# Kernel tuning notes

Measured on AMD Instinct MI355X. Metric: run time of the kernel, lower is better.

The kernel has to match this reference:

```python
import jax, jax.numpy as jnp
import numpy as np

GROUP_SIZE = 128

def setup_inputs() -> dict:
    key = jax.random.key(0)
    k0, k1, k2, k3 = jax.random.split(key, 4)
    B, S, K, N = 4, 16, 8192, 28672
    G = GROUP_SIZE
    x = jax.random.normal(k0, (B, S, K), dtype=jnp.float16)
    # packed uint8 stored as int32 (2 int4 nibbles per byte along K)
    w_packed = jax.random.randint(k1, (K // 2, N), 0, 256, dtype=jnp.int32)
    # per-group positive scales, typical magnitude for int4 quant of fp16 weights
    scales = (jax.random.uniform(k2, (K // G, N), dtype=jnp.float32) * 0.02 + 1e-4).astype(jnp.float16)
    bias = (jax.random.normal(k3, (N,), dtype=jnp.float16) * 0.02).astype(jnp.float16)
    return {"x": x, "w_packed": w_packed, "scales": scales, "bias": bias}

def _dequant(w_packed, scales):
    # w_packed: [K//2, N] ints in [0,256); low nibble -> even k, high nibble -> odd k
    low = (w_packed & 15) - 8          # [K//2, N] int32 in [-8, 7]
    high = ((w_packed >> 4) & 15) - 8  # [K//2, N]
    Kh, N = w_packed.shape
    w_int = jnp.stack([low, high], axis=1).reshape(Kh * 2, N)  # interleave -> [K, N]
    s = jnp.repeat(scales, GROUP_SIZE, axis=0)                 # [K, N] fp16
    return w_int.astype(jnp.float16) * s                       # [K, N] fp16

def reference(x, w_packed, scales, bias):
    # x: [B, S, K] fp16 -> y: [B, S, N] fp16
    w = _dequant(w_packed, scales)                 # [K, N] fp16
    lead = x.shape[:-1]
    x2 = x.reshape(-1, x.shape[-1])                # [M, K]
    # fp32 accumulation, fp16 output (matches Triton kernel's tl.dot accumulator)
    y = jnp.dot(x2, w, preferred_element_type=jnp.float32).astype(jnp.float16)
    y = y + bias
    return y.reshape(*lead, -1)
```

## Files before the change

### kernel.cpp

```cpp
#include <hip/hip_runtime.h>


typedef short  short8  __attribute__((ext_vector_type(8)));
typedef float  float4v __attribute__((ext_vector_type(4)));
typedef int    int4v   __attribute__((ext_vector_type(4)));
typedef unsigned int uint4v __attribute__((ext_vector_type(4)));

constexpr int Kd = 8192;
constexpr int Nd = 28672;
constexpr int KSPLIT = 4;

__device__ __forceinline__ unsigned f32_to_bf16_rn(float f) {
    unsigned u = __builtin_bit_cast(unsigned, f);
    return (u + 0x7FFFu + ((u >> 16) & 1u)) >> 16;
}

__device__ __forceinline__ void async16(const void* g, void* l) {
    __builtin_amdgcn_global_load_lds(
        (const __attribute__((address_space(1))) unsigned*)g,
        (__attribute__((address_space(3))) unsigned*)l, 16, 0, 0);
}

__global__ __launch_bounds__(256)
void init_y_kernel(const float* __restrict__ bias, float* __restrict__ y) {
    const int gid = blockIdx.x * 256 + threadIdx.x;
    const int m  = gid / (Nd / 4);
    const int nq = gid % (Nd / 4);
    ((float4v*)y)[(long)m * (Nd / 4) + nq] = ((const float4v*)bias)[nq];
}

__global__ __launch_bounds__(256)
void cvt_x_kernel(const float* __restrict__ x, unsigned short* __restrict__ o) {
    const int i = (blockIdx.x * 256 + threadIdx.x) * 8;
    float4v a = *(const float4v*)(x + i);
    float4v b = *(const float4v*)(x + i + 4);
    union { unsigned short s[8]; short8 v; } r;
    #pragma unroll
    for (int j = 0; j < 4; ++j) {
        r.s[j]     = (unsigned short)f32_to_bf16_rn(a[j]);
        r.s[4 + j] = (unsigned short)f32_to_bf16_rn(b[j]);
    }
    *(short8*)(o + i) = r.v;
}

__global__ __launch_bounds__(256, 4)
void int4_main_kernel(const unsigned short* __restrict__ xw,
                      const int*            __restrict__ wp,
                      const float*          __restrict__ scales,
                      float*                __restrict__ y)
{
    __shared__ unsigned wb0[2048], wb1[2048];
    __shared__ unsigned xb0[2048], xb1[2048];
    __shared__ unsigned sb[1024];

    const int t = threadIdx.x, lane = t & 63, wv = t >> 6;
    const int q = lane >> 4, c = lane & 15;
    const int l4 = lane >> 4, l15 = lane & 15;
    const int n0 = blockIdx.x * 64, kz = blockIdx.y;

    const int* wsrc0; const int* wsrc1;
    {
        int r0 = wv * 8 + 0 * 4 + l4, c0 = (l15 * 4) ^ (((wv * 2 + 0) & 3) << 4);
        int r1 = wv * 8 + 1 * 4 + l4, c1 = (l15 * 4) ^ (((wv * 2 + 1) & 3) << 4);
        wsrc0 = wp + (long)(kz * 1024 + r0) * Nd + n0 + c0;
        wsrc1 = wp + (long)(kz * 1024 + r1) * Nd + n0 + c1;
    }
    const unsigned short* xsrc0; const unsigned short* xsrc1;
    {
        int s0 = wv * 128 + 0 * 64 + lane, m0 = s0 >> 3, k0 = (s0 & 7) ^ (m0 & 7);
        int s1 = wv * 128 + 1 * 64 + lane, m1 = s1 >> 3, k1 = (s1 & 7) ^ (m1 & 7);
        xsrc0 = xw + (long)m0 * Kd + kz * 2048 + k0 * 8;
        xsrc1 = xw + (long)m1 * Kd + kz * 2048 + k1 * 8;
    }
    const int ldof = wv * 512;

    {
        const float* ssrc = scales + (long)(kz * 16 + (t >> 4)) * Nd + n0 + (t & 15) * 4;
        async16(ssrc, sb + wv * 256);
    }
    async16(wsrc0, wb0 + ldof);
    async16(wsrc1, wb0 + ldof + 256);
    async16(xsrc0, xb0 + ldof);
    async16(xsrc1, xb0 + ldof + 256);

    float4v acc[4] = {};

    auto stage = [&](int hg, unsigned* wbuf, unsigned* xbuf) {
        const long wof = (long)hg * 32 * Nd;
        const long xof = (long)hg * 64;
        async16(wsrc0 + wof, wbuf + ldof);
        async16(wsrc1 + wof, wbuf + ldof + 256);
        async16(xsrc0 + xof, xbuf + ldof);
        async16(xsrc1 + xof, xbuf + ldof + 256);
    };

    auto compute = [&](const unsigned* wbuf, const unsigned* xbuf, int g) {
        const float s   = __builtin_bit_cast(float, sb[g * 64 + wv * 16 + c]);
        const float m8s = -8.0f * s;
        #pragma unroll
        for (int it = 0; it < 2; ++it) {
            union { short8 h; unsigned u[4]; } bu;
            #pragma unroll
            for (int i = 0; i < 4; ++i) {
                unsigned v = wbuf[(it * 16 + q * 4 + i) * 64 + ((wv * 16 + c) ^ (q << 4))];
                float lo = fmaf((float)(v & 15u), s, m8s);
                float hi = fmaf((float)((v >> 4) & 15u), s, m8s);
                bu.u[i] = f32_to_bf16_rn(lo) | (f32_to_bf16_rn(hi) << 16);
            }
            #pragma unroll
            for (int mt = 0; mt < 4; ++mt) {
                int m = mt * 16 + c;
                int slot = m * 8 + ((it * 4 + q) ^ (c & 7));
                short8 a = *(const short8*)(xbuf + slot * 4);
                acc[mt] = __builtin_amdgcn_mfma_f32_16x16x32_bf16(a, bu.h, acc[mt], 0, 0, 0);
            }
        }
    };

    for (int hgp = 0; hgp < 16; ++hgp) {
        const int hg = 2 * hgp;
        stage(hg + 1, wb1, xb1);
        asm volatile("s_waitcnt vmcnt(4)\ns_barrier" ::: "memory");
        compute(wb0, xb0, hgp);
        asm volatile("s_waitcnt lgkmcnt(0)\ns_barrier" ::: "memory");
        if (hgp < 15) {
            stage(hg + 2, wb0, xb0);
            asm volatile("s_waitcnt vmcnt(4)\ns_barrier" ::: "memory");
        } else {
            asm volatile("s_waitcnt vmcnt(0)\ns_barrier" ::: "memory");
        }
        compute(wb1, xb1, hgp);
        asm volatile("s_waitcnt lgkmcnt(0)\ns_barrier" ::: "memory");
    }

    const int nw = n0 + wv * 16 + c;
    #pragma unroll
    for (int mt = 0; mt < 4; ++mt)
        #pragma unroll
        for (int r = 0; r < 4; ++r)
            atomicAdd(&y[(long)(mt * 16 + q * 4 + r) * Nd + nw], acc[mt][r]);
}

__global__ __launch_bounds__(256, 6)
void int4_main_nows_kernel(const float* __restrict__ xf,
                           const int*   __restrict__ wp,
                           const float* __restrict__ scales,
                           float*       __restrict__ y)
{
    constexpr int LDS_STRIDE = 68;
    __shared__ unsigned lds_w[64 * LDS_STRIDE];
    const int t = threadIdx.x, lane = t & 63, wv = t >> 6;
    const int q = lane >> 4, c = lane & 15;
    const int n0 = blockIdx.x * 64, kz = blockIdx.y;
    const int sr = t >> 4, ss = t & 15;
    const int*   wp_b = wp + (long)(kz * 1024 + sr) * Nd + n0 + 4 * ss;
    const float* sc_b = scales + (long)(kz * 16) * Nd + n0 + 4 * ss;
    const float* xf_b = xf + (long)c * Kd + kz * 2048 + q * 8;
    float4v acc[4] = {};

    for (int g = 0; g < 16; ++g) {
        const float4v s4 = *(const float4v*)(sc_b + (long)g * Nd);
        const int* wg = wp_b + (long)g * 64 * Nd;
        #pragma unroll
        for (int i = 0; i < 4; ++i) {
            int4v v = *(const int4v*)(wg + (long)i * 16 * Nd);
            uint4v pk;
            #pragma unroll
            for (int j = 0; j < 4; ++j) {
                float lo = (float)((v[j] & 15) - 8) * s4[j];
                float hi = (float)(((v[j] >> 4) & 15) - 8) * s4[j];
                pk[j] = f32_to_bf16_rn(lo) | (f32_to_bf16_rn(hi) << 16);
            }
            *(uint4v*)&lds_w[(i * 16 + sr) * LDS_STRIDE + 4 * ss] = pk;
        }
        __syncthreads();
        const float* xg = xf_b + g * 128;
        #pragma unroll
        for (int it = 0; it < 4; ++it) {
            union { short8 h; unsigned u[4]; } bu;
            #pragma unroll
            for (int i = 0; i < 4; ++i)
                bu.u[i] = lds_w[(it * 16 + q * 4 + i) * LDS_STRIDE + wv * 16 + c];
            const short8 b = bu.h;
            const float* xk = xg + it * 32;
            #pragma unroll
            for (int mt = 0; mt < 4; ++mt) {
                float4v a0 = *(const float4v*)(xk + (long)mt * 16 * Kd);
                float4v a1 = *(const float4v*)(xk + (long)mt * 16 * Kd + 4);
                union { unsigned short s[8]; short8 v; } r;
                #pragma unroll
                for (int j = 0; j < 4; ++j) {
                    r.s[j]     = (unsigned short)f32_to_bf16_rn(a0[j]);
                    r.s[4 + j] = (unsigned short)f32_to_bf16_rn(a1[j]);
                }
                acc[mt] = __builtin_amdgcn_mfma_f32_16x16x32_bf16(r.v, b, acc[mt], 0, 0, 0);
            }
        }
        __syncthreads();
    }
    const int nw = n0 + wv * 16 + c;
    #pragma unroll
    for (int mt = 0; mt < 4; ++mt)
        #pragma unroll
        for (int r = 0; r < 4; ++r)
            atomicAdd(&y[(long)(mt * 16 + q * 4 + r) * Nd + nw], acc[mt][r]);
}

extern "C" void kernel_launch(void* const* d_in, const int* in_sizes, int n_in,
                              void* d_out, int out_size, void* d_ws, size_t ws_size,
                              hipStream_t stream) {
    const float* x      = (const float*)d_in[0];
    const int*   wp     = (const int*)d_in[1];
    const float* scales = (const float*)d_in[2];
    const float* bias   = (const float*)d_in[3];
    float*       y      = (float*)d_out;

    init_y_kernel<<<dim3(1792), dim3(256), 0, stream>>>(bias, y);

    const size_t xb_bytes = (size_t)64 * Kd * sizeof(unsigned short);
    dim3 grid(Nd / 64, KSPLIT);
    dim3 block(256);

    if (ws_size >= xb_bytes) {
        unsigned short* xb = (unsigned short*)d_ws;
        cvt_x_kernel<<<dim3(256), dim3(256), 0, stream>>>(x, xb);
        int4_main_kernel<<<grid, block, 0, stream>>>(xb, wp, scales, y);
    } else {
        int4_main_nows_kernel<<<grid, block, 0, stream>>>(x, wp, scales, y);
    }
}
```

Baseline: 630.7 us.

## Switch int4 GEMM main loop to triple-buffered LDS with one barrier per step

```diff
diff --git a/kernel.cpp b/kernel.cpp
--- a/kernel.cpp
+++ b/kernel.cpp
@@ -43,14 +43,14 @@
     *(short8*)(o + i) = r.v;
 }
 
-__global__ __launch_bounds__(256, 4)
+__global__ __launch_bounds__(256, 3)
 void int4_main_kernel(const unsigned short* __restrict__ xw,
                       const int*            __restrict__ wp,
                       const float*          __restrict__ scales,
                       float*                __restrict__ y)
 {
-    __shared__ unsigned wb0[2048], wb1[2048];
-    __shared__ unsigned xb0[2048], xb1[2048];
+    __shared__ unsigned wbs[3][2048];
+    __shared__ unsigned xbs[3][2048];
     __shared__ unsigned sb[1024];
 
     const int t = threadIdx.x, lane = t & 63, wv = t >> 6;
@@ -73,17 +73,6 @@
         xsrc1 = xw + (long)m1 * Kd + kz * 2048 + k1 * 8;
     }
     const int ldof = wv * 512;
-
-    {
-        const float* ssrc = scales + (long)(kz * 16 + (t >> 4)) * Nd + n0 + (t & 15) * 4;
-        async16(ssrc, sb + wv * 256);
-    }
-    async16(wsrc0, wb0 + ldof);
-    async16(wsrc1, wb0 + ldof + 256);
-    async16(xsrc0, xb0 + ldof);
-    async16(xsrc1, xb0 + ldof + 256);
-
-    float4v acc[4] = {};
 
     auto stage = [&](int hg, unsigned* wbuf, unsigned* xbuf) {
         const long wof = (long)hg * 32 * Nd;
@@ -94,6 +83,8 @@
         async16(xsrc1 + xof, xbuf + ldof + 256);
     };
 
+    float4v acc[4] = {};
+
     auto compute = [&](const unsigned* wbuf, const unsigned* xbuf, int g) {
         const float s   = __builtin_bit_cast(float, sb[g * 64 + wv * 16 + c]);
         const float m8s = -8.0f * s;
@@ -117,21 +108,24 @@
         }
     };
 
-    for (int hgp = 0; hgp < 16; ++hgp) {
-        const int hg = 2 * hgp;
-        stage(hg + 1, wb1, xb1);
+    {
+        const float* ssrc = scales + (long)(kz * 16 + (t >> 4)) * Nd + n0 + (t & 15) * 4;
+        async16(ssrc, sb + wv * 256);
+    }
+    stage(0, wbs[0], xbs[0]);
+    stage(1, wbs[1], xbs[1]);
+
+    int cur = 0, nx2 = 2;
+    for (int i = 0; i < 31; ++i) {
         asm volatile("s_waitcnt vmcnt(4)\ns_barrier" ::: "memory");
-        compute(wb0, xb0, hgp);
-        asm volatile("s_waitcnt lgkmcnt(0)\ns_barrier" ::: "memory");
-        if (hgp < 15) {
-            stage(hg + 2, wb0, xb0);
-            asm volatile("s_waitcnt vmcnt(4)\ns_barrier" ::: "memory");
-        } else {
-            asm volatile("s_waitcnt vmcnt(0)\ns_barrier" ::: "memory");
-        }
-        compute(wb1, xb1, hgp);
-        asm volatile("s_waitcnt lgkmcnt(0)\ns_barrier" ::: "memory");
-    }
+        if (i < 30)
+            stage(i + 2, wbs[nx2], xbs[nx2]);
+        compute(wbs[cur], xbs[cur], i >> 1);
+        cur = (cur == 2) ? 0 : cur + 1;
+        nx2 = (nx2 == 2) ? 0 : nx2 + 1;
+    }
+    asm volatile("s_waitcnt vmcnt(0)\ns_barrier" ::: "memory");
+    compute(wbs[cur], xbs[cur], 15);
 
     const int nw = n0 + wv * 16 + c;
     #pragma unroll
```

After: 671.9 us. +6.5%, slower.
